# Performance work log

Hardware: AMD Instinct MI355X
Metric: run time of the kernel (lower is better)

The kernel has to match this reference:

```python
import jax, jax.numpy as jnp
import numpy as np

T = 200000


def _sine_layer(tvec, A, w, phi, phic, wc):
    # tvec: (t,), A/w/phi: (n,1), phic/wc: (1,)
    phi_static = jax.nn.relu(phic)  # (1,)
    w_static = jax.nn.relu(wc)
    ph = jax.nn.relu(phi) + phi_static  # (n,1)
    ww = jax.nn.relu(w) + w_static
    sine = A * jnp.sin(ww * tvec[None, :] + ph)  # (n,t)
    return sine, phi_static, w_static


def _selector_layer(tvec, wave_input, w, phi, phic, wc, phi_prev, w_prev):
    # wave_input: (n,t), w/phi: (m,n), phic/wc/phi_prev/w_prev: (1,)
    # NOTE: phi_prev/w_prev passed but phi_prev flag is False in the network,
    # so they are NOT added (matches torch: `if self.phi_prev and ...`).
    phi_static = jax.nn.relu(phic)
    w_static = jax.nn.relu(wc)
    ph = (jax.nn.relu(phi) + phi_static)[:, :, None]  # (m,n,1)
    ww = (jax.nn.relu(w) + w_static)[:, :, None]
    sine = 0.5 * jnp.sin(ww * tvec[None, None, :] + ph) + 0.5  # (m,n,t)
    out = jnp.einsum('mnt,nt->mt', sine, wave_input)  # (m,t)
    return out, phi_static, w_static


def setup_inputs() -> dict:
    key = jax.random.key(0)
    ks = jax.random.split(key, 18)
    r = lambda k, s: jax.random.normal(k, s, dtype=jnp.float32)
    return {
        'initial_wave_input': r(ks[0], (20, T)),
        'A0': r(ks[1], (20, 1)), 'w0': r(ks[2], (20, 1)), 'phi0': r(ks[3], (20, 1)),
        'wc0': r(ks[4], (1,)), 'phic0': r(ks[5], (1,)),
        'w1': r(ks[6], (25, 20)), 'phi1': r(ks[7], (25, 20)),
        'wc1': r(ks[8], (1,)), 'phic1': r(ks[9], (1,)),
        'w2': r(ks[10], (30, 25)), 'phi2': r(ks[11], (30, 25)),
        'wc2': r(ks[12], (1,)), 'phic2': r(ks[13], (1,)),
        'w3': r(ks[14], (1, 30)), 'phi3': r(ks[15], (1, 30)),
        'wc3': r(ks[16], (1,)), 'phic3': r(ks[17], (1,)),
    }


def reference(initial_wave_input, A0, w0, phi0, wc0, phic0,
              w1, phi1, wc1, phic1, w2, phi2, wc2, phic2,
              w3, phi3, wc3, phic3):
    tvec = jnp.linspace(1.0, 1000.0, T, dtype=jnp.float32)
    # initial_wave_input is an argument of the torch module but is never used.
    s, phi, w = _sine_layer(tvec, A0, w0, phi0, phic0, wc0)
    s, phi, w = _selector_layer(tvec, s, w1, phi1, phic1, wc1, phi, w)
    s, phi, w = _selector_layer(tvec, s, w2, phi2, phic2, wc2, phi, w)
    s, phi, w = _selector_layer(tvec, s, w3, phi3, phic3, wc3, phi, w)
    return s  # (1, t)
```

## Files before the change

### kernel.cpp

```cpp
#include <hip/hip_runtime.h>
#include <hip/hip_bf16.h>

#define T_TOTAL 200000

typedef float v4f __attribute__((ext_vector_type(4)));

__device__ float g_P[4512];

__device__ __forceinline__ float sinp(float rev) {
    float g = __builtin_amdgcn_fractf(rev);
    float h = g - 0.5f;
    float u = h * h;
    float p = fmaf(45.621248f, u, -82.391040f);
    p = fmaf(p, u, 64.671616f);
    p = fmaf(p, u, -19.730960f);
    p = fmaf(p, u, 0.9999618f);
    return p;
}

__global__ void prep_kernel(
    const float* __restrict__ A0,
    const float* __restrict__ w0, const float* __restrict__ phi0,
    const float* __restrict__ wc0, const float* __restrict__ phic0,
    const float* __restrict__ w1, const float* __restrict__ phi1,
    const float* __restrict__ wc1, const float* __restrict__ phic1,
    const float* __restrict__ w2, const float* __restrict__ phi2,
    const float* __restrict__ wc2, const float* __restrict__ phic2,
    const float* __restrict__ w3, const float* __restrict__ phi3,
    const float* __restrict__ wc3, const float* __restrict__ phic3)
{
    const int tid = blockIdx.x * blockDim.x + threadIdx.x;
    const int stride = blockDim.x * gridDim.x;

    const double I2PI = 0.15915494309189535;
    const double D64  = 64.0 * 999.0 / 199999.0;

    const double ws0 = fmax((double)wc0[0], 0.0), ps0 = fmax((double)phic0[0], 0.0);
    const double ws1 = fmax((double)wc1[0], 0.0), ps1 = fmax((double)phic1[0], 0.0);
    const double ws2 = fmax((double)wc2[0], 0.0), ps2 = fmax((double)phic2[0], 0.0);
    const double ws3 = fmax((double)wc3[0], 0.0), ps3 = fmax((double)phic3[0], 0.0);

    for (int n = tid; n < 24; n += stride) {
        float wwf = 0.0f, phf = 0.25f, cf = 2.0f, af = 0.0f;
        if (n < 20) {
            double wr = fmax((double)w0[n], 0.0) + ws0;
            wwf = (float)(wr * I2PI);
            phf = (float)((fmax((double)phi0[n], 0.0) + ps0) * I2PI + 0.25);
            cf  = (float)(2.0 * cos(wr * D64));
            af  = A0[n];
        }
        g_P[n]      = wwf;
        g_P[24 + n] = phf;
        g_P[48 + n] = cf;
        g_P[72 + n] = af;
    }
    for (int k = tid; k < 20 * 32; k += stride) {
        const int n = k >> 5, m = k & 31;
        float wwf = 0.0f, phf = 0.25f, cf = 2.0f;
        if (m < 25) {
            const int s = m * 20 + n;
            double wr = fmax((double)w1[s], 0.0) + ws1;
            wwf = (float)(wr * I2PI);
            phf = (float)((fmax((double)phi1[s], 0.0) + ps1) * I2PI + 0.25);
            cf  = (float)(2.0 * cos(wr * D64));
        }
        g_P[96 + 96 * n + m]      = wwf;
        g_P[96 + 96 * n + 32 + m] = phf;
        g_P[96 + 96 * n + 64 + m] = cf;
    }
    for (int k = tid; k < 25 * 32; k += stride) {
        const int n = k >> 5, m = k & 31;
        float wwf = 0.0f, phf = 0.25f, cf = 2.0f;
        if (m < 30) {
            const int s = m * 25 + n;
            double wr = fmax((double)w2[s], 0.0) + ws2;
            wwf = (float)(wr * I2PI);
            phf = (float)((fmax((double)phi2[s], 0.0) + ps2) * I2PI + 0.25);
            cf  = (float)(2.0 * cos(wr * D64));
        }
        g_P[2016 + 96 * n + m]      = wwf;
        g_P[2016 + 96 * n + 32 + m] = phf;
        g_P[2016 + 96 * n + 64 + m] = cf;
    }
    for (int k = tid; k < 32; k += stride) {
        float wwf = 0.0f, phf = 0.25f, cf = 2.0f;
        if (k < 30) {
            double wr = fmax((double)w3[k], 0.0) + ws3;
            wwf = (float)(wr * I2PI);
            phf = (float)((fmax((double)phi3[k], 0.0) + ps3) * I2PI + 0.25);
            cf  = (float)(2.0 * cos(wr * D64));
        }
        g_P[4416 + k]      = wwf;
        g_P[4416 + 32 + k] = phf;
        g_P[4416 + 64 + k] = cf;
    }
}

__launch_bounds__(512)
__global__ void wave_main(float* __restrict__ out)
{
    __shared__ float smem[12544];
    float* const sh0 = smem;
    float* const sh1 = smem + 6144;
    float* const shp = smem;

    const int l = threadIdx.x & 63;
    const int w = __builtin_amdgcn_readfirstlane(threadIdx.x >> 6);
    const int tb = blockIdx.x * 256;
    const float STEP = 999.0f / 199999.0f;

    float tv[4];
#pragma unroll
    for (int j = 0; j < 4; ++j)
        tv[j] = fmaf((float)(tb + l + 64 * j), STEP, 1.0f);

#pragma unroll
    for (int i = 0; i < 3; ++i) {
        const int n = 3 * w + i;
        const float ww = g_P[n], ph = g_P[24 + n], C = g_P[48 + n], A = g_P[72 + n];
        float x0 = A * sinp(fmaf(ww, tv[0], ph));
        float x1 = A * sinp(fmaf(ww, tv[1], ph));
        float x2 = fmaf(C, x1, -x0);
        float x3 = fmaf(C, x2, -x1);
        *(v4f*)&sh0[n * 256 + l * 4] = (v4f){x0, x1, x2, x3};
    }
    __syncthreads();

    float acc1[4][4] = {};
    float sum0[4] = {0.f, 0.f, 0.f, 0.f};
#pragma clang loop unroll(disable)
    for (int n = 0; n < 20; ++n) {
        const v4f s0 = *(const v4f*)&sh0[n * 256 + l * 4];
#pragma unroll
        for (int j = 0; j < 4; ++j) sum0[j] += s0[j];
        const float* __restrict__ pb = &g_P[96 + 96 * n + 4 * w];
#pragma unroll
        for (int k = 0; k < 4; ++k) {
            const float ww = pb[k], ph = pb[32 + k], C = pb[64 + k];
            float x0 = sinp(fmaf(ww, tv[0], ph));
            float x1 = sinp(fmaf(ww, tv[1], ph));
            float x2 = fmaf(C, x1, -x0);
            float x3 = fmaf(C, x2, -x1);
            acc1[k][0] = fmaf(x0, s0[0], acc1[k][0]);
            acc1[k][1] = fmaf(x1, s0[1], acc1[k][1]);
            acc1[k][2] = fmaf(x2, s0[2], acc1[k][2]);
            acc1[k][3] = fmaf(x3, s0[3], acc1[k][3]);
        }
    }
#pragma unroll
    for (int k = 0; k < 4; ++k) {
        if (4 * w + k < 25) {
            v4f v;
#pragma unroll
            for (int j = 0; j < 4; ++j) v[j] = fmaf(0.5f, acc1[k][j], 0.5f * sum0[j]);
            *(v4f*)&sh1[(4 * w + k) * 256 + l * 4] = v;
        }
    }
    __syncthreads();

    float acc2[4][4] = {};
    float sum1[4] = {0.f, 0.f, 0.f, 0.f};
#pragma clang loop unroll(disable)
    for (int n = 0; n < 25; ++n) {
        const v4f s1 = *(const v4f*)&sh1[n * 256 + l * 4];
#pragma unroll
        for (int j = 0; j < 4; ++j) sum1[j] += s1[j];
        const float* __restrict__ pb = &g_P[2016 + 96 * n + 4 * w];
#pragma unroll
        for (int k = 0; k < 4; ++k) {
            const float ww = pb[k], ph = pb[32 + k], C = pb[64 + k];
            float x0 = sinp(fmaf(ww, tv[0], ph));
            float x1 = sinp(fmaf(ww, tv[1], ph));
            float x2 = fmaf(C, x1, -x0);
            float x3 = fmaf(C, x2, -x1);
            acc2[k][0] = fmaf(x0, s1[0], acc2[k][0]);
            acc2[k][1] = fmaf(x1, s1[1], acc2[k][1]);
            acc2[k][2] = fmaf(x2, s1[2], acc2[k][2]);
            acc2[k][3] = fmaf(x3, s1[3], acc2[k][3]);
        }
    }
    float s2r[4][4];
#pragma unroll
    for (int k = 0; k < 4; ++k)
#pragma unroll
        for (int j = 0; j < 4; ++j)
            s2r[k][j] = fmaf(0.5f, acc2[k][j], 0.5f * sum1[j]);

    float pw[4] = {0.f, 0.f, 0.f, 0.f};
    {
        const float* __restrict__ pb = &g_P[4416 + 4 * w];
#pragma unroll
        for (int k = 0; k < 4; ++k) {
            if (4 * w + k < 30) {
                const float ww = pb[k], ph = pb[32 + k], C = pb[64 + k];
                float x0 = sinp(fmaf(ww, tv[0], ph));
                float x1 = sinp(fmaf(ww, tv[1], ph));
                float x2 = fmaf(C, x1, -x0);
                float x3 = fmaf(C, x2, -x1);
                pw[0] = fmaf(fmaf(0.5f, x0, 0.5f), s2r[k][0], pw[0]);
                pw[1] = fmaf(fmaf(0.5f, x1, 0.5f), s2r[k][1], pw[1]);
                pw[2] = fmaf(fmaf(0.5f, x2, 0.5f), s2r[k][2], pw[2]);
                pw[3] = fmaf(fmaf(0.5f, x3, 0.5f), s2r[k][3], pw[3]);
            }
        }
    }
    __syncthreads();
    *(v4f*)&shp[w * 256 + l * 4] = (v4f){pw[0], pw[1], pw[2], pw[3]};
    __syncthreads();

    if (w < 4) {
        float r = 0.0f;
#pragma unroll
        for (int w2 = 0; w2 < 8; ++w2)
            r += shp[w2 * 256 + l * 4 + w];
        const int tt = tb + l + 64 * w;
        if (tt < T_TOTAL) out[tt] = r;
    }
}

extern "C" void kernel_launch(void* const* d_in, const int* in_sizes, int n_in,
                              void* d_out, int out_size, void* d_ws, size_t ws_size,
                              hipStream_t stream) {
    (void)in_sizes; (void)n_in; (void)d_ws; (void)ws_size; (void)out_size;
    const float* A0    = (const float*)d_in[1];
    const float* w0    = (const float*)d_in[2];
    const float* phi0  = (const float*)d_in[3];
    const float* wc0   = (const float*)d_in[4];
    const float* phic0 = (const float*)d_in[5];
    const float* w1    = (const float*)d_in[6];
    const float* phi1  = (const float*)d_in[7];
    const float* wc1   = (const float*)d_in[8];
    const float* phic1 = (const float*)d_in[9];
    const float* w2    = (const float*)d_in[10];
    const float* phi2  = (const float*)d_in[11];
    const float* wc2   = (const float*)d_in[12];
    const float* phic2 = (const float*)d_in[13];
    const float* w3    = (const float*)d_in[14];
    const float* phi3  = (const float*)d_in[15];
    const float* wc3   = (const float*)d_in[16];
    const float* phic3 = (const float*)d_in[17];

    float* out = (float*)d_out;

    hipLaunchKernelGGL(prep_kernel, dim3(6), dim3(256), 0, stream,
                       A0, w0, phi0, wc0, phic0,
                       w1, phi1, wc1, phic1,
                       w2, phi2, wc2, phic2,
                       w3, phi3, wc3, phic3);

    const int grid = (T_TOTAL + 255) / 256;
    hipLaunchKernelGGL(wave_main, dim3(grid), dim3(512), 0, stream, out);
}
```

Before: 52.12 us.

## Recompute layer-0 sines per wave, prefetch params, drop a barrier and shared stage

Layer-0 sine values are no longer staged in shared memory. Each wave now recomputes them in registers inside the layer-1 loop, which removes one __syncthreads and the sh0 buffer. The parameter loads become vectorized v4f loads that are prefetched one iteration ahead in both selector loops, and the layer-0 parameters are repacked as interleaved quads. The final reduction buffer gets its own array with a conflict-free layout, which removes the barrier before its write. In exchange, every wave redundantly evaluates the 20 layer-0 sines, a small amount of extra ALU work, and the launch bounds now request 8 blocks per CU.

```diff
diff --git a/kernel.cpp b/kernel.cpp
--- a/kernel.cpp
+++ b/kernel.cpp
@@ -5,7 +5,7 @@
 
 typedef float v4f __attribute__((ext_vector_type(4)));
 
-__device__ float g_P[4512];
+__device__ float g_P[4496];
 
 __device__ __forceinline__ float sinp(float rev) {
     float g = __builtin_amdgcn_fractf(rev);
@@ -40,19 +40,12 @@
     const double ws2 = fmax((double)wc2[0], 0.0), ps2 = fmax((double)phic2[0], 0.0);
     const double ws3 = fmax((double)wc3[0], 0.0), ps3 = fmax((double)phic3[0], 0.0);
 
-    for (int n = tid; n < 24; n += stride) {
-        float wwf = 0.0f, phf = 0.25f, cf = 2.0f, af = 0.0f;
-        if (n < 20) {
-            double wr = fmax((double)w0[n], 0.0) + ws0;
-            wwf = (float)(wr * I2PI);
-            phf = (float)((fmax((double)phi0[n], 0.0) + ps0) * I2PI + 0.25);
-            cf  = (float)(2.0 * cos(wr * D64));
-            af  = A0[n];
-        }
-        g_P[n]      = wwf;
-        g_P[24 + n] = phf;
-        g_P[48 + n] = cf;
-        g_P[72 + n] = af;
+    for (int n = tid; n < 20; n += stride) {
+        double wr = fmax((double)w0[n], 0.0) + ws0;
+        g_P[4 * n]     = (float)(wr * I2PI);
+        g_P[4 * n + 1] = (float)((fmax((double)phi0[n], 0.0) + ps0) * I2PI + 0.25);
+        g_P[4 * n + 2] = (float)(2.0 * cos(wr * D64));
+        g_P[4 * n + 3] = A0[n];
     }
     for (int k = tid; k < 20 * 32; k += stride) {
         const int n = k >> 5, m = k & 31;
@@ -64,9 +57,9 @@
             phf = (float)((fmax((double)phi1[s], 0.0) + ps1) * I2PI + 0.25);
             cf  = (float)(2.0 * cos(wr * D64));
         }
-        g_P[96 + 96 * n + m]      = wwf;
-        g_P[96 + 96 * n + 32 + m] = phf;
-        g_P[96 + 96 * n + 64 + m] = cf;
+        g_P[80 + 96 * n + m]      = wwf;
+        g_P[80 + 96 * n + 32 + m] = phf;
+        g_P[80 + 96 * n + 64 + m] = cf;
     }
     for (int k = tid; k < 25 * 32; k += stride) {
         const int n = k >> 5, m = k & 31;
@@ -78,9 +71,9 @@
             phf = (float)((fmax((double)phi2[s], 0.0) + ps2) * I2PI + 0.25);
             cf  = (float)(2.0 * cos(wr * D64));
         }
-        g_P[2016 + 96 * n + m]      = wwf;
-        g_P[2016 + 96 * n + 32 + m] = phf;
-        g_P[2016 + 96 * n + 64 + m] = cf;
+        g_P[2000 + 96 * n + m]      = wwf;
+        g_P[2000 + 96 * n + 32 + m] = phf;
+        g_P[2000 + 96 * n + 64 + m] = cf;
     }
     for (int k = tid; k < 32; k += stride) {
         float wwf = 0.0f, phf = 0.25f, cf = 2.0f;
@@ -90,61 +83,58 @@
             phf = (float)((fmax((double)phi3[k], 0.0) + ps3) * I2PI + 0.25);
             cf  = (float)(2.0 * cos(wr * D64));
         }
-        g_P[4416 + k]      = wwf;
-        g_P[4416 + 32 + k] = phf;
-        g_P[4416 + 64 + k] = cf;
-    }
-}
-
-__launch_bounds__(512)
+        g_P[4400 + k]      = wwf;
+        g_P[4400 + 32 + k] = phf;
+        g_P[4400 + 64 + k] = cf;
+    }
+}
+
+__launch_bounds__(512, 8)
 __global__ void wave_main(float* __restrict__ out)
 {
-    __shared__ float smem[12544];
-    float* const sh0 = smem;
-    float* const sh1 = smem + 6144;
-    float* const shp = smem;
+    __shared__ float sh1[26 * 256];
+    __shared__ float shp[8 * 256];
 
     const int l = threadIdx.x & 63;
     const int w = __builtin_amdgcn_readfirstlane(threadIdx.x >> 6);
     const int tb = blockIdx.x * 256;
     const float STEP = 999.0f / 199999.0f;
 
-    float tv[4];
-#pragma unroll
-    for (int j = 0; j < 4; ++j)
-        tv[j] = fmaf((float)(tb + l + 64 * j), STEP, 1.0f);
-
-#pragma unroll
-    for (int i = 0; i < 3; ++i) {
-        const int n = 3 * w + i;
-        const float ww = g_P[n], ph = g_P[24 + n], C = g_P[48 + n], A = g_P[72 + n];
-        float x0 = A * sinp(fmaf(ww, tv[0], ph));
-        float x1 = A * sinp(fmaf(ww, tv[1], ph));
-        float x2 = fmaf(C, x1, -x0);
-        float x3 = fmaf(C, x2, -x1);
-        *(v4f*)&sh0[n * 256 + l * 4] = (v4f){x0, x1, x2, x3};
-    }
-    __syncthreads();
+    const float tv0 = fmaf((float)(tb + l), STEP, 1.0f);
+    const float tv1 = fmaf((float)(tb + l + 64), STEP, 1.0f);
 
     float acc1[4][4] = {};
     float sum0[4] = {0.f, 0.f, 0.f, 0.f};
+    {
+        v4f qN  = *(const v4f*)&g_P[0];
+        v4f wwN = *(const v4f*)&g_P[80 + 4 * w];
+        v4f phN = *(const v4f*)&g_P[80 + 32 + 4 * w];
+        v4f CN  = *(const v4f*)&g_P[80 + 64 + 4 * w];
 #pragma clang loop unroll(disable)
-    for (int n = 0; n < 20; ++n) {
-        const v4f s0 = *(const v4f*)&sh0[n * 256 + l * 4];
-#pragma unroll
-        for (int j = 0; j < 4; ++j) sum0[j] += s0[j];
-        const float* __restrict__ pb = &g_P[96 + 96 * n + 4 * w];
-#pragma unroll
-        for (int k = 0; k < 4; ++k) {
-            const float ww = pb[k], ph = pb[32 + k], C = pb[64 + k];
-            float x0 = sinp(fmaf(ww, tv[0], ph));
-            float x1 = sinp(fmaf(ww, tv[1], ph));
-            float x2 = fmaf(C, x1, -x0);
-            float x3 = fmaf(C, x2, -x1);
-            acc1[k][0] = fmaf(x0, s0[0], acc1[k][0]);
-            acc1[k][1] = fmaf(x1, s0[1], acc1[k][1]);
-            acc1[k][2] = fmaf(x2, s0[2], acc1[k][2]);
-            acc1[k][3] = fmaf(x3, s0[3], acc1[k][3]);
+        for (int n = 0; n < 20; ++n) {
+            const v4f q = qN, ww4 = wwN, ph4 = phN, C4 = CN;
+            qN  = *(const v4f*)&g_P[4 * (n + 1)];
+            const float* __restrict__ pn = &g_P[80 + 96 * (n + 1) + 4 * w];
+            wwN = *(const v4f*)&pn[0];
+            phN = *(const v4f*)&pn[32];
+            CN  = *(const v4f*)&pn[64];
+
+            float s00 = q[3] * sinp(fmaf(q[0], tv0, q[1]));
+            float s01 = q[3] * sinp(fmaf(q[0], tv1, q[1]));
+            float s02 = fmaf(q[2], s01, -s00);
+            float s03 = fmaf(q[2], s02, -s01);
+            sum0[0] += s00; sum0[1] += s01; sum0[2] += s02; sum0[3] += s03;
+#pragma unroll
+            for (int k = 0; k < 4; ++k) {
+                float x0 = sinp(fmaf(ww4[k], tv0, ph4[k]));
+                float x1 = sinp(fmaf(ww4[k], tv1, ph4[k]));
+                float x2 = fmaf(C4[k], x1, -x0);
+                float x3 = fmaf(C4[k], x2, -x1);
+                acc1[k][0] = fmaf(x0, s00, acc1[k][0]);
+                acc1[k][1] = fmaf(x1, s01, acc1[k][1]);
+                acc1[k][2] = fmaf(x2, s02, acc1[k][2]);
+                acc1[k][3] = fmaf(x3, s03, acc1[k][3]);
+            }
         }
     }
 #pragma unroll
@@ -160,23 +150,32 @@
 
     float acc2[4][4] = {};
     float sum1[4] = {0.f, 0.f, 0.f, 0.f};
+    {
+        v4f s1N = *(const v4f*)&sh1[l * 4];
+        v4f wwN = *(const v4f*)&g_P[2000 + 4 * w];
+        v4f phN = *(const v4f*)&g_P[2000 + 32 + 4 * w];
+        v4f CN  = *(const v4f*)&g_P[2000 + 64 + 4 * w];
 #pragma clang loop unroll(disable)
-    for (int n = 0; n < 25; ++n) {
-        const v4f s1 = *(const v4f*)&sh1[n * 256 + l * 4];
-#pragma unroll
-        for (int j = 0; j < 4; ++j) sum1[j] += s1[j];
-        const float* __restrict__ pb = &g_P[2016 + 96 * n + 4 * w];
-#pragma unroll
-        for (int k = 0; k < 4; ++k) {
-            const float ww = pb[k], ph = pb[32 + k], C = pb[64 + k];
-            float x0 = sinp(fmaf(ww, tv[0], ph));
-            float x1 = sinp(fmaf(ww, tv[1], ph));
-            float x2 = fmaf(C, x1, -x0);
-            float x3 = fmaf(C, x2, -x1);
-            acc2[k][0] = fmaf(x0, s1[0], acc2[k][0]);
-            acc2[k][1] = fmaf(x1, s1[1], acc2[k][1]);
-            acc2[k][2] = fmaf(x2, s1[2], acc2[k][2]);
-            acc2[k][3] = fmaf(x3, s1[3], acc2[k][3]);
+        for (int n = 0; n < 25; ++n) {
+            const v4f s1 = s1N, ww4 = wwN, ph4 = phN, C4 = CN;
+            s1N = *(const v4f*)&sh1[(n + 1) * 256 + l * 4];
+            const float* __restrict__ pn = &g_P[2000 + 96 * (n + 1) + 4 * w];
+            wwN = *(const v4f*)&pn[0];
+            phN = *(const v4f*)&pn[32];
+            CN  = *(const v4f*)&pn[64];
+
+            sum1[0] += s1[0]; sum1[1] += s1[1]; sum1[2] += s1[2]; sum1[3] += s1[3];
+#pragma unroll
+            for (int k = 0; k < 4; ++k) {
+                float x0 = sinp(fmaf(ww4[k], tv0, ph4[k]));
+                float x1 = sinp(fmaf(ww4[k], tv1, ph4[k]));
+                float x2 = fmaf(C4[k], x1, -x0);
+                float x3 = fmaf(C4[k], x2, -x1);
+                acc2[k][0] = fmaf(x0, s1[0], acc2[k][0]);
+                acc2[k][1] = fmaf(x1, s1[1], acc2[k][1]);
+                acc2[k][2] = fmaf(x2, s1[2], acc2[k][2]);
+                acc2[k][3] = fmaf(x3, s1[3], acc2[k][3]);
+            }
         }
     }
     float s2r[4][4];
@@ -188,13 +187,13 @@
 
     float pw[4] = {0.f, 0.f, 0.f, 0.f};
     {
-        const float* __restrict__ pb = &g_P[4416 + 4 * w];
+        const float* __restrict__ pb = &g_P[4400 + 4 * w];
 #pragma unroll
         for (int k = 0; k < 4; ++k) {
             if (4 * w + k < 30) {
                 const float ww = pb[k], ph = pb[32 + k], C = pb[64 + k];
-                float x0 = sinp(fmaf(ww, tv[0], ph));
-                float x1 = sinp(fmaf(ww, tv[1], ph));
+                float x0 = sinp(fmaf(ww, tv0, ph));
+                float x1 = sinp(fmaf(ww, tv1, ph));
                 float x2 = fmaf(C, x1, -x0);
                 float x3 = fmaf(C, x2, -x1);
                 pw[0] = fmaf(fmaf(0.5f, x0, 0.5f), s2r[k][0], pw[0]);
@@ -204,15 +203,16 @@
             }
         }
     }
-    __syncthreads();
-    *(v4f*)&shp[w * 256 + l * 4] = (v4f){pw[0], pw[1], pw[2], pw[3]};
+#pragma unroll
+    for (int j = 0; j < 4; ++j)
+        shp[w * 256 + j * 64 + l] = pw[j];
     __syncthreads();
 
     if (w < 4) {
         float r = 0.0f;
 #pragma unroll
         for (int w2 = 0; w2 < 8; ++w2)
-            r += shp[w2 * 256 + l * 4 + w];
+            r += shp[w2 * 256 + w * 64 + l];
         const int tt = tb + l + 64 * w;
         if (tt < T_TOTAL) out[tt] = r;
     }
```

After: 56.27 us. +8.0%, slower.
